# Performance work log

Measured on AMD Instinct MI355X. Metric: run time of the kernel, lower is better.

The kernel has to match this reference:

```python
import jax, jax.numpy as jnp
import numpy as np
import math

SCALE = math.sqrt(256.0)

def setup_inputs() -> dict:
    key = jax.random.key(0)
    k1, k2, k3, k4, k5 = jax.random.split(key, 5)
    B, C, T, D = 8, 80, 2048, 256
    bound = 1.0 / math.sqrt(C)
    x = jax.random.normal(k1, (B, C, T), dtype=jnp.float32)
    Wk = jax.random.uniform(k2, (D, C), minval=-bound, maxval=bound, dtype=jnp.float32)
    bk = jax.random.uniform(k3, (D,), minval=-bound, maxval=bound, dtype=jnp.float32)
    Wq = jax.random.uniform(k4, (D, C), minval=-bound, maxval=bound, dtype=jnp.float32)
    bq = jax.random.uniform(k5, (D,), minval=-bound, maxval=bound, dtype=jnp.float32)
    return {"x": x, "Wk": Wk, "bk": bk, "Wq": Wq, "bq": bq}

def reference(x, Wk, bk, Wq, bq):
    # x: [B, C=80, T]; work in time-major layout [B, T, C]
    xt = jnp.swapaxes(x, 1, 2)                      # [B, T, C]
    K = xt @ Wk.T + bk                              # [B, T, 256]
    Q = xt @ Wq.T + bq                              # [B, T, 256]
    # softmax over last dim (dim=2 in torch) of K Q^T / sqrt(256)
    att = jax.nn.softmax(jnp.einsum('bid,bjd->bij', K, Q) / SCALE, axis=2)
    # original per-timestep loop is exactly att @ xt (values = raw input, no V proj)
    out = jnp.einsum('bij,bjc->bic', att, xt)       # [B, T, C]
    return jnp.swapaxes(out, 1, 2)                  # [B, C, T]
```

## Files before the change

kernel.cpp:

```cpp
#include <hip/hip_runtime.h>
#include <hip/hip_bf16.h>
#include <math.h>

typedef __bf16 bf16;
typedef __bf16 bf16x8 __attribute__((ext_vector_type(8)));
typedef float  f32x4  __attribute__((ext_vector_type(4)));
typedef float  f32x16 __attribute__((ext_vector_type(16)));
typedef uint32_t u32x4 __attribute__((ext_vector_type(4)));

#define MFMA16(a, b, c) __builtin_amdgcn_mfma_f32_16x16x32_bf16((a), (b), (c), 0, 0, 0)
#define MFMA32(a, b, c) __builtin_amdgcn_mfma_f32_32x32x16_bf16((a), (b), (c), 0, 0, 0)

typedef const uint32_t __attribute__((address_space(1)))* gq_t;
typedef uint32_t __attribute__((address_space(3)))* lq_t;

constexpr int B_ = 8, C_ = 80, T_ = 2048, D_ = 256;
constexpr int NS = 4;
constexpr float SCALE_INV = 1.0f / 16.0f;

static __device__ inline uint32_t pkbf(float lo, float hi) {
  bf16 l = (bf16)lo, h = (bf16)hi;
  uint16_t lb = __builtin_bit_cast(uint16_t, l), hb = __builtin_bit_cast(uint16_t, h);
  return (uint32_t)lb | ((uint32_t)hb << 16);
}

__global__ __launch_bounds__(256) void proj_kernel(
    const float* __restrict__ x,
    const float* __restrict__ Wk,
    const float* __restrict__ bk,
    const float* __restrict__ Wq,
    const float* __restrict__ bq,
    bf16* __restrict__ Kb,
    bf16* __restrict__ Qb,
    bf16* __restrict__ xbf)
{
  const int t0   = blockIdx.x * 32;
  const int b    = blockIdx.y;
  const int tid  = threadIdx.x;
  const int w    = tid >> 6;
  const int lane = tid & 63;
  const int h    = lane >> 4;
  const int lr   = lane & 15;

  const float* xb = x + (size_t)b * C_ * T_;

  {
    bf16* ob = xbf + (size_t)b * C_ * T_;
    #pragma unroll
    for (int q = 0; q < 10; ++q) {
      int idx = q * 256 + tid;
      int c = idx >> 5, tt = idx & 31;
      ob[c * T_ + t0 + tt] = (bf16)xb[c * T_ + t0 + tt];
    }
  }

  bf16x8 afrag[2][3];
  #pragma unroll
  for (int ib = 0; ib < 2; ++ib) {
    int t = t0 + ib * 16 + lr;
    #pragma unroll
    for (int ks = 0; ks < 3; ++ks) {
      bf16x8 v;
      #pragma unroll
      for (int e = 0; e < 8; ++e) {
        int c = ks * 32 + h * 8 + e;
        float val;
        if (c < 80)       val = xb[c * T_ + t];
        else if (c == 80) val = 1.0f;
        else              val = 0.0f;
        v[e] = (bf16)val;
      }
      afrag[ib][ks] = v;
    }
  }

  const int nb0 = w * 4;
  #pragma unroll
  for (int mat = 0; mat < 2; ++mat) {
    const float* W    = mat ? Wq : Wk;
    const float* bias = mat ? bq : bk;
    bf16* outp        = mat ? Qb : Kb;

    f32x4 acc[2][4];
    #pragma unroll
    for (int ib = 0; ib < 2; ++ib)
      #pragma unroll
      for (int nb = 0; nb < 4; ++nb)
        acc[ib][nb] = f32x4{0.f, 0.f, 0.f, 0.f};

    #pragma unroll
    for (int nb = 0; nb < 4; ++nb) {
      int d = (nb0 + nb) * 16 + lr;
      #pragma unroll
      for (int ks = 0; ks < 3; ++ks) {
        bf16x8 bv;
        #pragma unroll
        for (int e = 0; e < 8; ++e) {
          int c = ks * 32 + h * 8 + e;
          float val;
          if (c < 80)       val = W[d * C_ + c];
          else if (c == 80) val = bias[d];
          else              val = 0.0f;
          bv[e] = (bf16)val;
        }
        #pragma unroll
        for (int ib = 0; ib < 2; ++ib)
          acc[ib][nb] = MFMA16(afrag[ib][ks], bv, acc[ib][nb]);
      }
    }

    #pragma unroll
    for (int ib = 0; ib < 2; ++ib)
      #pragma unroll
      for (int nb = 0; nb < 4; ++nb) {
        int d = (nb0 + nb) * 16 + lr;
        #pragma unroll
        for (int r = 0; r < 4; ++r) {
          int t = t0 + ib * 16 + h * 4 + r;
          outp[(size_t)(b * T_ + t) * D_ + d] = (bf16)acc[ib][nb][r];
        }
      }
  }
}

__global__ __launch_bounds__(256, 2) void attn_kernel(
    const bf16* __restrict__ Kb,
    const bf16* __restrict__ Qb,
    const bf16* __restrict__ xbf,
    float* __restrict__ Opart,
    float* __restrict__ mpart,
    float* __restrict__ lpart)
{
  constexpr int BN = 32, NT = T_ / BN;
  constexpr int JT_PER = NT / NS;
  __shared__ bf16 qlds[2][BN * D_];

  const int flat = blockIdx.x;
  const int b    = flat & 7;
  const int rem  = flat >> 3;
  const int it   = rem & 15;
  const int s    = rem >> 4;
  const int i0   = it * 128;

  const int tid  = threadIdx.x;
  const int w    = tid >> 6;
  const int lane = tid & 63;
  const int il   = lane & 31;
  const int hi   = lane >> 5;
  const int iw   = i0 + w * 32;

  const bf16* Kbase = Kb  + (size_t)b * T_ * D_;
  const bf16* Qbase = Qb  + (size_t)b * T_ * D_;
  const bf16* Vbase = xbf + (size_t)b * C_ * T_;

  bf16x8 kf[16];
  {
    const bf16* kp = Kbase + (size_t)(iw + il) * D_ + hi * 8;
    #pragma unroll
    for (int ks = 0; ks < 16; ++ks)
      kf[ks] = *reinterpret_cast<const bf16x8*>(kp + ks * 16);
  }

  f32x16 oacc[3];
  #pragma unroll
  for (int cb = 0; cb < 3; ++cb)
    #pragma unroll
    for (int r = 0; r < 16; ++r) oacc[cb][r] = 0.f;
  float m_run = -INFINITY, l_run = 0.f;

  auto stage = [&](int jt, int buf) {
    #pragma unroll
    for (int q = 0; q < 4; ++q) {
      int f = tid + 256 * q;
      int j = f >> 5, c = f & 31;
      const bf16* src = Qbase + (size_t)(jt * BN + j) * D_ + ((c ^ j) << 3);
      __builtin_amdgcn_global_load_lds((gq_t)src,
          (lq_t)&qlds[buf][(q * 256 + w * 64) * 8], 16, 0, 0);
    }
  };

  const int jt0 = s * JT_PER, jtend = jt0 + JT_PER;

  stage(jt0, 0);
  asm volatile("s_waitcnt vmcnt(0)" ::: "memory");
  __syncthreads();

  int cur = 0;
  for (int jt = jt0; jt < jtend; ++jt, cur ^= 1) {
    if (jt + 1 < jtend) stage(jt + 1, cur ^ 1);

    bf16x8 vf[3][2];
    #pragma unroll
    for (int cb = 0; cb < 3; ++cb)
      #pragma unroll
      for (int kj = 0; kj < 2; ++kj)
        vf[cb][kj] = *reinterpret_cast<const bf16x8*>(
            Vbase + (size_t)(cb * 32 + il) * T_ + jt * BN + hi * 8 + kj * 16);

    f32x16 sacc;
    #pragma unroll
    for (int r = 0; r < 16; ++r) sacc[r] = 0.f;
    __builtin_amdgcn_s_setprio(1);
    #pragma unroll
    for (int ks = 0; ks < 16; ++ks) {
      bf16x8 qa = *reinterpret_cast<const bf16x8*>(
          &qlds[cur][il * 256 + (((hi + 2 * ks) ^ il) << 3)]);
      sacc = MFMA32(qa, kf[ks], sacc);
    }
    __builtin_amdgcn_s_setprio(0);

    float p16[16];
    #pragma unroll
    for (int r = 0; r < 16; ++r) p16[r] = sacc[r];
    float mx = p16[0];
    #pragma unroll
    for (int r = 1; r < 16; ++r) mx = fmaxf(mx, p16[r]);
    mx = fmaxf(mx, __shfl_xor(mx, 32));

    if (!__all(mx <= m_run + 48.f)) {
      float mnew  = fmaxf(m_run, mx);
      float alpha = __expf((m_run - mnew) * SCALE_INV);
      m_run = mnew;
      l_run *= alpha;
      #pragma unroll
      for (int cb = 0; cb < 3; ++cb)
        #pragma unroll
        for (int r = 0; r < 16; ++r) oacc[cb][r] *= alpha;
    }
    float rs = 0.f;
    #pragma unroll
    for (int r = 0; r < 16; ++r) {
      p16[r] = __expf((p16[r] - m_run) * SCALE_INV);
      rs += p16[r];
    }
    rs += __shfl_xor(rs, 32);
    l_run += rs;

    uint32_t a0 = pkbf(p16[0],  p16[1]),  a1 = pkbf(p16[2],  p16[3]);
    uint32_t c0 = pkbf(p16[4],  p16[5]),  c1 = pkbf(p16[6],  p16[7]);
    uint32_t a2 = pkbf(p16[8],  p16[9]),  a3 = pkbf(p16[10], p16[11]);
    uint32_t c2 = pkbf(p16[12], p16[13]), c3 = pkbf(p16[14], p16[15]);
    uint32_t a0s = __shfl_xor(a0, 32), a1s = __shfl_xor(a1, 32);
    uint32_t c0s = __shfl_xor(c0, 32), c1s = __shfl_xor(c1, 32);
    uint32_t a2s = __shfl_xor(a2, 32), a3s = __shfl_xor(a3, 32);
    uint32_t c2s = __shfl_xor(c2, 32), c3s = __shfl_xor(c3, 32);
    const bool h = (hi != 0);
    u32x4 pb0 = { h ? c0s : a0, h ? c1s : a1, h ? c0 : a0s, h ? c1 : a1s };
    u32x4 pb1 = { h ? c2s : a2, h ? c3s : a3, h ? c2 : a2s, h ? c3 : a3s };
    bf16x8 pbf0 = __builtin_bit_cast(bf16x8, pb0);
    bf16x8 pbf1 = __builtin_bit_cast(bf16x8, pb1);

    __builtin_amdgcn_s_setprio(1);
    #pragma unroll
    for (int cb = 0; cb < 3; ++cb) {
      oacc[cb] = MFMA32(vf[cb][0], pbf0, oacc[cb]);
      oacc[cb] = MFMA32(vf[cb][1], pbf1, oacc[cb]);
    }
    __builtin_amdgcn_s_setprio(0);

    asm volatile("s_waitcnt vmcnt(0)" ::: "memory");
    __syncthreads();
  }

  float* ob = Opart + (size_t)(s * B_ + b) * C_ * T_;
  #pragma unroll
  for (int cb = 0; cb < 3; ++cb)
    #pragma unroll
    for (int r = 0; r < 16; ++r) {
      if (cb < 2 || r < 8) {
        int c = cb * 32 + (r & 3) + 8 * (r >> 2) + 4 * hi;
        ob[(size_t)c * T_ + iw + il] = oacc[cb][r];
      }
    }
  if (lane < 32) {
    mpart[(size_t)(s * B_ + b) * T_ + iw + il] = m_run;
    lpart[(size_t)(s * B_ + b) * T_ + iw + il] = l_run;
  }
}

__global__ __launch_bounds__(256) void merge_kernel(
    const float* __restrict__ Opart,
    const float* __restrict__ mpart,
    const float* __restrict__ lpart,
    float* __restrict__ out)
{
  const int b    = blockIdx.y;
  const int tid  = threadIdx.x;
  const int w    = tid >> 6;
  const int lane = tid & 63;
  const int t    = blockIdx.x * 64 + lane;

  float m[NS];
  float mmax = -INFINITY;
  #pragma unroll
  for (int s2 = 0; s2 < NS; ++s2) {
    m[s2] = mpart[(size_t)(s2 * B_ + b) * T_ + t];
    mmax = fmaxf(mmax, m[s2]);
  }
  float e[NS];
  float lsum = 0.f;
  #pragma unroll
  for (int s2 = 0; s2 < NS; ++s2) {
    e[s2] = __expf((m[s2] - mmax) * SCALE_INV);
    lsum += e[s2] * lpart[(size_t)(s2 * B_ + b) * T_ + t];
  }
  const float inv = 1.0f / lsum;

  const int c0 = w * 20;
  for (int c = c0; c < c0 + 20; ++c) {
    float acc = 0.f;
    #pragma unroll
    for (int s2 = 0; s2 < NS; ++s2)
      acc += Opart[((size_t)(s2 * B_ + b) * C_ + c) * T_ + t] * e[s2];
    out[((size_t)b * C_ + c) * T_ + t] = acc * inv;
  }
}

extern "C" void kernel_launch(void* const* d_in, const int* in_sizes, int n_in,
                              void* d_out, int out_size, void* d_ws, size_t ws_size,
                              hipStream_t stream) {
  (void)in_sizes; (void)n_in; (void)out_size; (void)ws_size;
  const float* x  = (const float*)d_in[0];
  const float* Wk = (const float*)d_in[1];
  const float* bk = (const float*)d_in[2];
  const float* Wq = (const float*)d_in[3];
  const float* bq = (const float*)d_in[4];
  float* out = (float*)d_out;

  char* ws = (char*)d_ws;
  const size_t MB = 1024 * 1024;
  bf16*  Kb    = (bf16*)(ws);
  bf16*  Qb    = (bf16*)(ws + 8 * MB);
  bf16*  xbf   = (bf16*)(ws + 16 * MB);
  float* Opart = (float*)(ws + 19 * MB);
  float* mpart = (float*)(ws + 41 * MB);
  float* lpart = (float*)(ws + 42 * MB);

  dim3 blk(256);
  dim3 g1(T_ / 32, B_);
  proj_kernel<<<g1, blk, 0, stream>>>(x, Wk, bk, Wq, bq, Kb, Qb, xbf);
  attn_kernel<<<dim3(16 * NS * B_), blk, 0, stream>>>(Kb, Qb, xbf, Opart, mpart, lpart);
  dim3 g3(T_ / 64, B_);
  merge_kernel<<<g3, blk, 0, stream>>>(Opart, mpart, lpart, out);
}
```

Measured before the change: 68.20 us.

## Vectorize conversion and merge loads, split QK accumulator chain, use exp2

The x-to-bf16 conversion in the projection kernel now uses 16-byte vector loads and stores, and the merge kernel handles four timesteps per thread with f32x4 loads and stores. In the attention loop, the QK^T MFMA chain is split across two accumulators that are summed at the end, which shortens the dependency chain. The row max becomes a tree reduction, and exp uses exp2f with a prescaled log2e/16 constant. The aim is to cut memory instruction count and MFMA dependency stalls, at the cost of more registers for the second accumulator.

```diff
diff --git a/kernel.cpp b/kernel.cpp
--- a/kernel.cpp
+++ b/kernel.cpp
@@ -16,7 +16,7 @@
 
 constexpr int B_ = 8, C_ = 80, T_ = 2048, D_ = 256;
 constexpr int NS = 4;
-constexpr float SCALE_INV = 1.0f / 16.0f;
+constexpr float LOG2E_16 = 0.090169989f;
 
 static __device__ inline uint32_t pkbf(float lo, float hi) {
   bf16 l = (bf16)lo, h = (bf16)hi;
@@ -46,12 +46,16 @@
 
   {
     bf16* ob = xbf + (size_t)b * C_ * T_;
-    #pragma unroll
-    for (int q = 0; q < 10; ++q) {
-      int idx = q * 256 + tid;
-      int c = idx >> 5, tt = idx & 31;
-      ob[c * T_ + t0 + tt] = (bf16)xb[c * T_ + t0 + tt];
-    }
+    auto conv8 = [&](int c, int ch) {
+      const f32x4* sp = reinterpret_cast<const f32x4*>(xb + (size_t)c * T_ + t0 + ch * 8);
+      f32x4 v0 = sp[0], v1 = sp[1];
+      bf16x8 o;
+      #pragma unroll
+      for (int e = 0; e < 4; ++e) { o[e] = (bf16)v0[e]; o[e + 4] = (bf16)v1[e]; }
+      *reinterpret_cast<bf16x8*>(ob + (size_t)c * T_ + t0 + ch * 8) = o;
+    };
+    conv8(tid >> 2, tid & 3);
+    if (tid < 64) conv8(64 + (tid >> 2), tid & 3);
   }
 
   bf16x8 afrag[2][3];
@@ -197,29 +201,40 @@
         vf[cb][kj] = *reinterpret_cast<const bf16x8*>(
             Vbase + (size_t)(cb * 32 + il) * T_ + jt * BN + hi * 8 + kj * 16);
 
-    f32x16 sacc;
-    #pragma unroll
-    for (int r = 0; r < 16; ++r) sacc[r] = 0.f;
+    f32x16 s0, s1;
+    #pragma unroll
+    for (int r = 0; r < 16; ++r) { s0[r] = 0.f; s1[r] = 0.f; }
     __builtin_amdgcn_s_setprio(1);
     #pragma unroll
-    for (int ks = 0; ks < 16; ++ks) {
-      bf16x8 qa = *reinterpret_cast<const bf16x8*>(
+    for (int ks = 0; ks < 16; ks += 2) {
+      bf16x8 qa0 = *reinterpret_cast<const bf16x8*>(
           &qlds[cur][il * 256 + (((hi + 2 * ks) ^ il) << 3)]);
-      sacc = MFMA32(qa, kf[ks], sacc);
+      bf16x8 qa1 = *reinterpret_cast<const bf16x8*>(
+          &qlds[cur][il * 256 + (((hi + 2 * (ks + 1)) ^ il) << 3)]);
+      s0 = MFMA32(qa0, kf[ks], s0);
+      s1 = MFMA32(qa1, kf[ks + 1], s1);
     }
     __builtin_amdgcn_s_setprio(0);
+    f32x16 sacc = s0 + s1;
 
     float p16[16];
     #pragma unroll
     for (int r = 0; r < 16; ++r) p16[r] = sacc[r];
-    float mx = p16[0];
-    #pragma unroll
-    for (int r = 1; r < 16; ++r) mx = fmaxf(mx, p16[r]);
+    float mx01 = fmaxf(p16[0], p16[1]);
+    float mx23 = fmaxf(p16[2], p16[3]);
+    float mx45 = fmaxf(p16[4], p16[5]);
+    float mx67 = fmaxf(p16[6], p16[7]);
+    float mx89 = fmaxf(p16[8], p16[9]);
+    float mxab = fmaxf(p16[10], p16[11]);
+    float mxcd = fmaxf(p16[12], p16[13]);
+    float mxef = fmaxf(p16[14], p16[15]);
+    float mx = fmaxf(fmaxf(fmaxf(mx01, mx23), fmaxf(mx45, mx67)),
+                     fmaxf(fmaxf(mx89, mxab), fmaxf(mxcd, mxef)));
     mx = fmaxf(mx, __shfl_xor(mx, 32));
 
     if (!__all(mx <= m_run + 48.f)) {
       float mnew  = fmaxf(m_run, mx);
-      float alpha = __expf((m_run - mnew) * SCALE_INV);
+      float alpha = exp2f((m_run - mnew) * LOG2E_16);
       m_run = mnew;
       l_run *= alpha;
       #pragma unroll
@@ -230,7 +245,7 @@
     float rs = 0.f;
     #pragma unroll
     for (int r = 0; r < 16; ++r) {
-      p16[r] = __expf((p16[r] - m_run) * SCALE_INV);
+      p16[r] = exp2f((p16[r] - m_run) * LOG2E_16);
       rs += p16[r];
     }
     rs += __shfl_xor(rs, 32);
@@ -244,9 +259,9 @@
     uint32_t c0s = __shfl_xor(c0, 32), c1s = __shfl_xor(c1, 32);
     uint32_t a2s = __shfl_xor(a2, 32), a3s = __shfl_xor(a3, 32);
     uint32_t c2s = __shfl_xor(c2, 32), c3s = __shfl_xor(c3, 32);
-    const bool h = (hi != 0);
-    u32x4 pb0 = { h ? c0s : a0, h ? c1s : a1, h ? c0 : a0s, h ? c1 : a1s };
-    u32x4 pb1 = { h ? c2s : a2, h ? c3s : a3, h ? c2 : a2s, h ? c3 : a3s };
+    const bool hh = (hi != 0);
+    u32x4 pb0 = { hh ? c0s : a0, hh ? c1s : a1, hh ? c0 : a0s, hh ? c1 : a1s };
+    u32x4 pb1 = { hh ? c2s : a2, hh ? c3s : a3, hh ? c2 : a2s, hh ? c3 : a3s };
     bf16x8 pbf0 = __builtin_bit_cast(bf16x8, pb0);
     bf16x8 pbf1 = __builtin_bit_cast(bf16x8, pb1);
 
@@ -284,35 +299,44 @@
     const float* __restrict__ lpart,
     float* __restrict__ out)
 {
-  const int b    = blockIdx.y;
-  const int tid  = threadIdx.x;
-  const int w    = tid >> 6;
-  const int lane = tid & 63;
-  const int t    = blockIdx.x * 64 + lane;
-
-  float m[NS];
-  float mmax = -INFINITY;
+  const int b      = blockIdx.y;
+  const int tid    = threadIdx.x;
+  const int slot   = tid & 15;
+  const int cstrip = tid >> 4;
+  const int t4     = blockIdx.x * 64 + slot * 4;
+
+  f32x4 m[NS], e[NS];
+  f32x4 mmax;
+  #pragma unroll
+  for (int s2 = 0; s2 < NS; ++s2)
+    m[s2] = *reinterpret_cast<const f32x4*>(&mpart[(size_t)(s2 * B_ + b) * T_ + t4]);
+  #pragma unroll
+  for (int r = 0; r < 4; ++r) {
+    mmax[r] = m[0][r];
+    #pragma unroll
+    for (int s2 = 1; s2 < NS; ++s2) mmax[r] = fmaxf(mmax[r], m[s2][r]);
+  }
+  f32x4 lsum = f32x4{0.f, 0.f, 0.f, 0.f};
   #pragma unroll
   for (int s2 = 0; s2 < NS; ++s2) {
-    m[s2] = mpart[(size_t)(s2 * B_ + b) * T_ + t];
-    mmax = fmaxf(mmax, m[s2]);
-  }
-  float e[NS];
-  float lsum = 0.f;
-  #pragma unroll
-  for (int s2 = 0; s2 < NS; ++s2) {
-    e[s2] = __expf((m[s2] - mmax) * SCALE_INV);
-    lsum += e[s2] * lpart[(size_t)(s2 * B_ + b) * T_ + t];
-  }
-  const float inv = 1.0f / lsum;
-
-  const int c0 = w * 20;
-  for (int c = c0; c < c0 + 20; ++c) {
-    float acc = 0.f;
+    f32x4 lv = *reinterpret_cast<const f32x4*>(&lpart[(size_t)(s2 * B_ + b) * T_ + t4]);
+    #pragma unroll
+    for (int r = 0; r < 4; ++r) e[s2][r] = exp2f((m[s2][r] - mmax[r]) * LOG2E_16);
+    lsum += e[s2] * lv;
+  }
+  f32x4 inv;
+  #pragma unroll
+  for (int r = 0; r < 4; ++r) inv[r] = 1.0f / lsum[r];
+
+  #pragma unroll
+  for (int cc = 0; cc < 5; ++cc) {
+    const int c = cstrip * 5 + cc;
+    f32x4 acc = f32x4{0.f, 0.f, 0.f, 0.f};
     #pragma unroll
     for (int s2 = 0; s2 < NS; ++s2)
-      acc += Opart[((size_t)(s2 * B_ + b) * C_ + c) * T_ + t] * e[s2];
-    out[((size_t)b * C_ + c) * T_ + t] = acc * inv;
+      acc += *reinterpret_cast<const f32x4*>(
+                 &Opart[((size_t)(s2 * B_ + b) * C_ + c) * T_ + t4]) * e[s2];
+    *reinterpret_cast<f32x4*>(&out[((size_t)b * C_ + c) * T_ + t4]) = acc * inv;
   }
 }
 
```

Measured after the change: 70.63 us. 1.04x slower.
